# Optimization experiments

Hardware: AMD Instinct MI355X
Metric: run time of the kernel (lower is better)

## Reference

```python
import jax, jax.numpy as jnp
import numpy as np

K = 1  # number of items to sample exactly
B, N = 512, 8192


def log1mexp(x):
    # log(1 - exp(x)) for x <= 0, numerically stable (Maechler 2012)
    return jnp.where(x > -jnp.log(2.0), jnp.log(-jnp.expm1(x)), jnp.log1p(-jnp.exp(x)))


def logaddexp_c(x1, x2):
    # custom logaddexp matching the torch module (handles -inf == -inf ties)
    delta = jnp.where(x1 == x2, 0.0, x1 - x2)
    return jnp.maximum(x1, x2) + jax.nn.softplus(-jnp.abs(delta))


def dp_table(logp, logq, kk):
    # a[b, i, c] = log Pr(exactly c-1 successes among first i items); shape [B, n+1, kk+2]
    bsz = logp.shape[0]
    state0 = jnp.full((bsz, kk + 2), -jnp.inf, logp.dtype).at[:, 1].set(0.0)
    ninf_col = jnp.full((bsz, 1), -jnp.inf, logp.dtype)

    def step(state, xs):
        lp, lq = xs  # each [B]
        grown = logaddexp_c(state[:, :-1] + lp[:, None], state[:, 1:] + lq[:, None])
        new = jnp.concatenate([ninf_col, grown], axis=1)
        return new, new

    _, rows = jax.lax.scan(step, state0, (logp.T, logq.T))  # rows: [n, B, kk+2]
    return jnp.concatenate([state0[None], rows], axis=0).transpose(1, 0, 2)


def sample_scan(a, logp, noise):
    # reverse DP sampling pass; a: [B, n+1, C], logp/noise: [B, n]
    bsz, np1, C = a.shape
    n = np1 - 1
    kcol = C - 1  # == K + 1 in table-column coordinates
    ap = a[:, :-1, :][:, ::-1].transpose(1, 0, 2)  # [n, B, C], row i-1 for i=n..1
    ac = a[:, 1:, :][:, ::-1].transpose(1, 0, 2)   # [n, B, C], row i   for i=n..1
    lp_rev = logp[:, ::-1].T                        # [n, B]
    u_rev = noise[:, ::-1].T                        # [n, B]

    def step(j, xs):
        ap_r, ac_r, lp_t, u_t = xs
        p = jnp.take_along_axis(ap_r, (j - 1)[:, None], axis=1)[:, 0]
        z = jnp.take_along_axis(ac_r, j[:, None], axis=1)[:, 0]
        p = jnp.minimum(p + lp_t - z, 0.0)  # conditional log-prob, clamp fp round-off
        q = log1mexp(p)
        X = (u_t < jax.nn.sigmoid(p - q)).astype(logp.dtype)  # Bernoulli(logits=p-q)
        j = jnp.where(X > 0, j - 1, j)
        return j, X

    j0 = jnp.full((bsz,), kcol, jnp.int32)
    _, Xs = jax.lax.scan(step, j0, (ap, ac, lp_rev, u_rev))  # Xs: [n, B]
    return Xs[::-1].T  # [B, n]


def setup_inputs() -> dict:
    key = jax.random.key(0)
    k1, k2 = jax.random.split(key)
    logits = jax.random.normal(k1, (B, N), dtype=jnp.float32)
    noise = jax.random.uniform(k2, (B, N), dtype=jnp.float32)
    return {"logits": logits, "noise": noise}


def reference(logits, noise):
    logp = jnp.minimum(jax.nn.log_sigmoid(logits), -1e-7)  # clamped log_sigmoid
    logq = log1mexp(logp)
    a = dp_table(logp, logq, K)       # [B, N+1, K+2]
    return sample_scan(a, logp, noise)  # [B, N] in {0,1}
```

## Files before the change

### kernel.cpp

```cpp
#include <hip/hip_runtime.h>
#include <math.h>

#define NB 512
#define NI 8192
#define NG (NI / 4)
#define NLOG2 0.69314718055994530942f

__device__ __forceinline__ float log1mexp_f(float x) {
    return (x > -NLOG2) ? logf(-expm1f(x)) : log1pf(-expf(x));
}

__device__ int g_sel[NB];

#define TB 64
#define TK 16
__global__ __launch_bounds__(256) void prep_kernel(const float* __restrict__ logits,
                                                   float* __restrict__ Alp,
                                                   float* __restrict__ Blq) {
    __shared__ float4 lp_t[TB][TK + 1];
    __shared__ float4 lq_t[TB][TK + 1];
    int bx = blockIdx.x;
    int tb = (bx & 7) * TB;
    int tkb = (bx >> 3) * TK;
    int t = threadIdx.x;

    int kl = t & 15;
    int rl0 = t >> 4;
#pragma unroll
    for (int r = 0; r < 4; ++r) {
        int row_local = r * 16 + rl0;
        float4 x4 = *(const float4*)&logits[(size_t)(tb + row_local) * NI + (size_t)(tkb + kl) * 4];
        float4 lp4, lq4;
        const float* xs = &x4.x;
        float* lps = &lp4.x;
        float* lqs = &lq4.x;
#pragma unroll
        for (int j = 0; j < 4; ++j) {
            float x = xs[j];
            float lp = -(fmaxf(-x, 0.0f) + log1pf(expf(-fabsf(x))));
            lp = fminf(lp, -1e-7f);
            lps[j] = lp;
            lqs[j] = log1mexp_f(lp);
        }
        lp_t[row_local][kl] = lp4;
        lq_t[row_local][kl] = lq4;
    }
    __syncthreads();

    int bl = t & 63;
    int kw0 = t >> 6;
#pragma unroll
    for (int w = 0; w < 4; ++w) {
        int k_local = w * 4 + kw0;
        size_t dst = (size_t)(tkb + k_local) * NB + (size_t)(tb + bl);
        ((float4*)Alp)[dst] = lp_t[bl][k_local];
        ((float4*)Blq)[dst] = lq_t[bl][k_local];
    }
}

__device__ __forceinline__ void scan_step(float lp, float lq, float& S0, float& S1,
                                          float& x1o, float& s1o) {
    const float L2E = 1.44269504088896340736f;
    const float LN2 = 0.69314718055994530942f;
    float x1 = S0 + lp;
    float x2 = S1 + lq;
    float d  = x1 - x2;
    float m  = fmaxf(x1, x2);
    float z  = fabsf(d) * -L2E;
    float e  = __builtin_amdgcn_exp2f(z);
    float a  = 1.0f + e;
    float l  = __builtin_amdgcn_logf(a);
    S1 = fmaf(l, LN2, m);
    S0 = S0 + lq;
    x1o = x1;
    s1o = S1;
}

__device__ __forceinline__ void scan_step4(float4 lp, float4 lq, float& S0, float& S1,
                                           float4& x1v, float4& s1v) {
    scan_step(lp.x, lq.x, S0, S1, x1v.x, s1v.x);
    scan_step(lp.y, lq.y, S0, S1, x1v.y, s1v.y);
    scan_step(lp.z, lq.z, S0, S1, x1v.z, s1v.z);
    scan_step(lp.w, lq.w, S0, S1, x1v.w, s1v.w);
}

#define SD 8
__global__ __launch_bounds__(64, 1) void scan_kernel(float* __restrict__ A,
                                                     float* __restrict__ B) {
    int row = blockIdx.x * 64 + threadIdx.x;
    float4* Ap = (float4*)A;
    float4* Bp = (float4*)B;

    float S0 = 0.0f;
    float S1 = -INFINITY;

    float4 lpA[SD], lqA[SD], lpB[SD], lqB[SD];

#pragma unroll
    for (int j = 0; j < SD; ++j) {
        lpA[j] = Ap[(size_t)j * NB + row];
        lqA[j] = Bp[(size_t)j * NB + row];
    }

    const int NCHUNK = NG / SD;
    for (int c = 0; c < NCHUNK; c += 2) {
        size_t g1 = (size_t)(c + 1) * SD;
        size_t g2 = (size_t)(c + 2) * SD;

#pragma unroll
        for (int j = 0; j < SD; ++j) {
            lpB[j] = Ap[(g1 + j) * NB + row];
            lqB[j] = Bp[(g1 + j) * NB + row];
        }

#pragma unroll
        for (int j = 0; j < SD; ++j) {
            float4 x1v, s1v;
            scan_step4(lpA[j], lqA[j], S0, S1, x1v, s1v);
            size_t g = (size_t)c * SD + j;
            Ap[g * NB + row] = x1v;
            Bp[g * NB + row] = s1v;
        }

        if (c + 2 < NCHUNK) {
#pragma unroll
            for (int j = 0; j < SD; ++j) {
                lpA[j] = Ap[(g2 + j) * NB + row];
                lqA[j] = Bp[(g2 + j) * NB + row];
            }
        }

#pragma unroll
        for (int j = 0; j < SD; ++j) {
            float4 x1v, s1v;
            scan_step4(lpB[j], lqB[j], S0, S1, x1v, s1v);
            size_t g = g1 + j;
            Ap[g * NB + row] = x1v;
            Bp[g * NB + row] = s1v;
        }
    }
}

__global__ __launch_bounds__(256) void decide_kernel(const float* __restrict__ A,
                                                     const float* __restrict__ S,
                                                     const float* __restrict__ noise) {
    int row = blockIdx.x;
    const float4* x1p = (const float4*)A;
    const float4* s1p = (const float4*)S;
    const float4* ur = (const float4*)(noise + (size_t)row * NI);
    int tid = threadIdx.x;

    int best = -1;
#pragma unroll
    for (int k = 0; k < NG / 256; ++k) {
        int g = tid + k * 256;
        float4 x1 = x1p[(size_t)g * NB + row];
        float4 s1 = s1p[(size_t)g * NB + row];
        float4 u = ur[g];
#pragma unroll
        for (int j = 0; j < 4; ++j) {
            float p = fminf((&x1.x)[j] - (&s1.x)[j], 0.0f);
            float q = log1mexp_f(p);
            float z = p - q;
            float prob = 1.0f / (1.0f + expf(-z));
            if ((&u.x)[j] < prob) {
                int i = 4 * g + j;
                best = (i > best) ? i : best;
            }
        }
    }

#pragma unroll
    for (int off = 32; off > 0; off >>= 1) {
        int o = __shfl_down(best, off);
        best = (o > best) ? o : best;
    }
    __shared__ int lds[4];
    int wid = tid >> 6;
    if ((tid & 63) == 0) lds[wid] = best;
    __syncthreads();
    if (tid == 0) {
        int s01 = (lds[0] > lds[1]) ? lds[0] : lds[1];
        int s23 = (lds[2] > lds[3]) ? lds[2] : lds[3];
        g_sel[row] = (s01 > s23) ? s01 : s23;
    }
}

__global__ __launch_bounds__(256) void writeout_kernel(float* __restrict__ out) {
    int row = blockIdx.x;
    int sel = g_sel[row];
    float4* outr = (float4*)(out + (size_t)row * NI);
    int tid = threadIdx.x;
#pragma unroll
    for (int k = 0; k < NG / 256; ++k) {
        int g = tid + k * 256;
        int i0 = 4 * g;
        float4 v;
        v.x = (i0 == sel) ? 1.0f : 0.0f;
        v.y = (i0 + 1 == sel) ? 1.0f : 0.0f;
        v.z = (i0 + 2 == sel) ? 1.0f : 0.0f;
        v.w = (i0 + 3 == sel) ? 1.0f : 0.0f;
        outr[g] = v;
    }
}

extern "C" void kernel_launch(void* const* d_in, const int* in_sizes, int n_in,
                              void* d_out, int out_size, void* d_ws, size_t ws_size,
                              hipStream_t stream) {
    (void)in_sizes; (void)n_in; (void)out_size; (void)ws_size;
    const float* logits = (const float*)d_in[0];
    const float* noise = (const float*)d_in[1];
    float* out = (float*)d_out;
    float* A = (float*)d_ws;

    prep_kernel<<<8 * (NG / TK), 256, 0, stream>>>(logits, A, out);
    scan_kernel<<<8, 64, 0, stream>>>(A, out);
    decide_kernel<<<NB, 256, 0, stream>>>(A, out, noise);
    writeout_kernel<<<NB, 256, 0, stream>>>(out);
}
```

Before: 408.2 us.

## Interleave two independent row scans per thread and store only conditional log-probs

Each scan thread now handles two rows, row and row+256, and interleaves their dependent logaddexp chains so one row's latency is hidden by the other's work. The grid shrinks from 8 to 4 wavefronts. The scan also computes the clamped conditional log-prob x1 - S1 itself and writes one array instead of two, which halves scan stores and halves the decide kernel's loads. The risk is that half as many wavefronts occupy the GPU, so a latency-bound serial scan may slow down if two-way ILP does not make up for the lost parallelism.

```diff
diff --git a/kernel.cpp b/kernel.cpp
--- a/kernel.cpp
+++ b/kernel.cpp
@@ -58,8 +58,8 @@
     }
 }
 
-__device__ __forceinline__ void scan_step(float lp, float lq, float& S0, float& S1,
-                                          float& x1o, float& s1o) {
+__device__ __forceinline__ void scan_step_p(float lp, float lq, float& S0, float& S1,
+                                            float& po) {
     const float L2E = 1.44269504088896340736f;
     const float LN2 = 0.69314718055994530942f;
     float x1 = S0 + lp;
@@ -72,34 +72,29 @@
     float l  = __builtin_amdgcn_logf(a);
     S1 = fmaf(l, LN2, m);
     S0 = S0 + lq;
-    x1o = x1;
-    s1o = S1;
-}
-
-__device__ __forceinline__ void scan_step4(float4 lp, float4 lq, float& S0, float& S1,
-                                           float4& x1v, float4& s1v) {
-    scan_step(lp.x, lq.x, S0, S1, x1v.x, s1v.x);
-    scan_step(lp.y, lq.y, S0, S1, x1v.y, s1v.y);
-    scan_step(lp.z, lq.z, S0, S1, x1v.z, s1v.z);
-    scan_step(lp.w, lq.w, S0, S1, x1v.w, s1v.w);
-}
-
-#define SD 8
+    po = fminf(x1 - S1, 0.0f);
+}
+
+#define SD 4
 __global__ __launch_bounds__(64, 1) void scan_kernel(float* __restrict__ A,
                                                      float* __restrict__ B) {
     int row = blockIdx.x * 64 + threadIdx.x;
+    int row1 = row + 256;
     float4* Ap = (float4*)A;
     float4* Bp = (float4*)B;
 
-    float S0 = 0.0f;
-    float S1 = -INFINITY;
-
-    float4 lpA[SD], lqA[SD], lpB[SD], lqB[SD];
+    float S0a = 0.0f, S1a = -INFINITY;
+    float S0b = 0.0f, S1b = -INFINITY;
+
+    float4 lpA0[SD], lqA0[SD], lpA1[SD], lqA1[SD];
+    float4 lpB0[SD], lqB0[SD], lpB1[SD], lqB1[SD];
 
 #pragma unroll
     for (int j = 0; j < SD; ++j) {
-        lpA[j] = Ap[(size_t)j * NB + row];
-        lqA[j] = Bp[(size_t)j * NB + row];
+        lpA0[j] = Ap[(size_t)j * NB + row];
+        lqA0[j] = Bp[(size_t)j * NB + row];
+        lpA1[j] = Ap[(size_t)j * NB + row1];
+        lqA1[j] = Bp[(size_t)j * NB + row1];
     }
 
     const int NCHUNK = NG / SD;
@@ -109,44 +104,59 @@
 
 #pragma unroll
         for (int j = 0; j < SD; ++j) {
-            lpB[j] = Ap[(g1 + j) * NB + row];
-            lqB[j] = Bp[(g1 + j) * NB + row];
+            lpB0[j] = Ap[(g1 + j) * NB + row];
+            lqB0[j] = Bp[(g1 + j) * NB + row];
+            lpB1[j] = Ap[(g1 + j) * NB + row1];
+            lqB1[j] = Bp[(g1 + j) * NB + row1];
         }
 
 #pragma unroll
         for (int j = 0; j < SD; ++j) {
-            float4 x1v, s1v;
-            scan_step4(lpA[j], lqA[j], S0, S1, x1v, s1v);
+            float4 p0, p1;
+            scan_step_p(lpA0[j].x, lqA0[j].x, S0a, S1a, p0.x);
+            scan_step_p(lpA1[j].x, lqA1[j].x, S0b, S1b, p1.x);
+            scan_step_p(lpA0[j].y, lqA0[j].y, S0a, S1a, p0.y);
+            scan_step_p(lpA1[j].y, lqA1[j].y, S0b, S1b, p1.y);
+            scan_step_p(lpA0[j].z, lqA0[j].z, S0a, S1a, p0.z);
+            scan_step_p(lpA1[j].z, lqA1[j].z, S0b, S1b, p1.z);
+            scan_step_p(lpA0[j].w, lqA0[j].w, S0a, S1a, p0.w);
+            scan_step_p(lpA1[j].w, lqA1[j].w, S0b, S1b, p1.w);
             size_t g = (size_t)c * SD + j;
-            Ap[g * NB + row] = x1v;
-            Bp[g * NB + row] = s1v;
+            Ap[g * NB + row] = p0;
+            Ap[g * NB + row1] = p1;
         }
 
         if (c + 2 < NCHUNK) {
 #pragma unroll
             for (int j = 0; j < SD; ++j) {
-                lpA[j] = Ap[(g2 + j) * NB + row];
-                lqA[j] = Bp[(g2 + j) * NB + row];
+                lpA0[j] = Ap[(g2 + j) * NB + row];
+                lqA0[j] = Bp[(g2 + j) * NB + row];
+                lpA1[j] = Ap[(g2 + j) * NB + row1];
+                lqA1[j] = Bp[(g2 + j) * NB + row1];
             }
         }
 
 #pragma unroll
         for (int j = 0; j < SD; ++j) {
-            float4 x1v, s1v;
-            scan_step4(lpB[j], lqB[j], S0, S1, x1v, s1v);
-            size_t g = g1 + j;
-            Ap[g * NB + row] = x1v;
-            Bp[g * NB + row] = s1v;
-        }
-    }
-}
-
-__global__ __launch_bounds__(256) void decide_kernel(const float* __restrict__ A,
-                                                     const float* __restrict__ S,
+            float4 p0, p1;
+            scan_step_p(lpB0[j].x, lqB0[j].x, S0a, S1a, p0.x);
+            scan_step_p(lpB1[j].x, lqB1[j].x, S0b, S1b, p1.x);
+            scan_step_p(lpB0[j].y, lqB0[j].y, S0a, S1a, p0.y);
+            scan_step_p(lpB1[j].y, lqB1[j].y, S0b, S1b, p1.y);
+            scan_step_p(lpB0[j].z, lqB0[j].z, S0a, S1a, p0.z);
+            scan_step_p(lpB1[j].z, lqB1[j].z, S0b, S1b, p1.z);
+            scan_step_p(lpB0[j].w, lqB0[j].w, S0a, S1a, p0.w);
+            scan_step_p(lpB1[j].w, lqB1[j].w, S0b, S1b, p1.w);
+            Ap[(g1 + j) * NB + row] = p0;
+            Ap[(g1 + j) * NB + row1] = p1;
+        }
+    }
+}
+
+__global__ __launch_bounds__(256) void decide_kernel(const float* __restrict__ P,
                                                      const float* __restrict__ noise) {
     int row = blockIdx.x;
-    const float4* x1p = (const float4*)A;
-    const float4* s1p = (const float4*)S;
+    const float4* pp = (const float4*)P;
     const float4* ur = (const float4*)(noise + (size_t)row * NI);
     int tid = threadIdx.x;
 
@@ -154,12 +164,11 @@
 #pragma unroll
     for (int k = 0; k < NG / 256; ++k) {
         int g = tid + k * 256;
-        float4 x1 = x1p[(size_t)g * NB + row];
-        float4 s1 = s1p[(size_t)g * NB + row];
+        float4 p4 = pp[(size_t)g * NB + row];
         float4 u = ur[g];
 #pragma unroll
         for (int j = 0; j < 4; ++j) {
-            float p = fminf((&x1.x)[j] - (&s1.x)[j], 0.0f);
+            float p = (&p4.x)[j];
             float q = log1mexp_f(p);
             float z = p - q;
             float prob = 1.0f / (1.0f + expf(-z));
@@ -214,7 +223,7 @@
     float* A = (float*)d_ws;
 
     prep_kernel<<<8 * (NG / TK), 256, 0, stream>>>(logits, A, out);
-    scan_kernel<<<8, 64, 0, stream>>>(A, out);
-    decide_kernel<<<NB, 256, 0, stream>>>(A, out, noise);
+    scan_kernel<<<4, 64, 0, stream>>>(A, out);
+    decide_kernel<<<NB, 256, 0, stream>>>(A, noise);
     writeout_kernel<<<NB, 256, 0, stream>>>(out);
 }
```

Result: slower. 734.7 us (+80.0%).

## Emit clamped conditional log-prob from scan and fuse decide with writeout

Applied to the files above, without the earlier changes.

The scan kernel now computes the clamped conditional log-probability p = min(x1 - S1, 0) itself and writes a single float per item to a separate global buffer, instead of writing both x1 and S1 back in place. This halves the scan's store traffic and the decide kernel's loads. The writeout kernel is folded into decide, with the selected index broadcast through shared memory, which removes one launch and a global round trip. The scan also uses sched_barrier fences and wraparound prefetch indices that do redundant loads in the last iterations, and the new 16 MB device-global buffer adds memory footprint.

```diff
diff --git a/kernel.cpp b/kernel.cpp
--- a/kernel.cpp
+++ b/kernel.cpp
@@ -1,5 +1,6 @@
 #include <hip/hip_runtime.h>
 #include <math.h>
+#include <stdint.h>
 
 #define NB 512
 #define NI 8192
@@ -10,7 +11,7 @@
     return (x > -NLOG2) ? logf(-expm1f(x)) : log1pf(-expf(x));
 }
 
-__device__ int g_sel[NB];
+__device__ float g_P[(size_t)NB * NI];
 
 #define TB 64
 #define TK 16
@@ -58,8 +59,8 @@
     }
 }
 
-__device__ __forceinline__ void scan_step(float lp, float lq, float& S0, float& S1,
-                                          float& x1o, float& s1o) {
+__device__ __forceinline__ void scan_step_p(float lp, float lq, float& S0, float& S1,
+                                            float& po) {
     const float L2E = 1.44269504088896340736f;
     const float LN2 = 0.69314718055994530942f;
     float x1 = S0 + lp;
@@ -72,94 +73,93 @@
     float l  = __builtin_amdgcn_logf(a);
     S1 = fmaf(l, LN2, m);
     S0 = S0 + lq;
-    x1o = x1;
-    s1o = S1;
-}
-
-__device__ __forceinline__ void scan_step4(float4 lp, float4 lq, float& S0, float& S1,
-                                           float4& x1v, float4& s1v) {
-    scan_step(lp.x, lq.x, S0, S1, x1v.x, s1v.x);
-    scan_step(lp.y, lq.y, S0, S1, x1v.y, s1v.y);
-    scan_step(lp.z, lq.z, S0, S1, x1v.z, s1v.z);
-    scan_step(lp.w, lq.w, S0, S1, x1v.w, s1v.w);
-}
-
-#define SD 8
-__global__ __launch_bounds__(64, 1) void scan_kernel(float* __restrict__ A,
-                                                     float* __restrict__ B) {
+    po = fminf(x1 - S1, 0.0f);
+}
+
+#define CH 8
+#define SB() __builtin_amdgcn_sched_barrier(0)
+
+__global__ __launch_bounds__(64, 1) void scan_kernel(const float* __restrict__ A,
+                                                     const float* __restrict__ B) {
     int row = blockIdx.x * 64 + threadIdx.x;
-    float4* Ap = (float4*)A;
-    float4* Bp = (float4*)B;
-
-    float S0 = 0.0f;
-    float S1 = -INFINITY;
-
-    float4 lpA[SD], lqA[SD], lpB[SD], lqB[SD];
-
-#pragma unroll
-    for (int j = 0; j < SD; ++j) {
-        lpA[j] = Ap[(size_t)j * NB + row];
-        lqA[j] = Bp[(size_t)j * NB + row];
-    }
-
-    const int NCHUNK = NG / SD;
+    const float4* Ap = (const float4*)A;
+    const float4* Bp = (const float4*)B;
+    float4* Pp = (float4*)g_P;
+
+    float S0 = 0.0f, S1 = -INFINITY;
+    float4 lpE[CH], lqE[CH], lpO[CH], lqO[CH];
+
+#pragma unroll
+    for (int j = 0; j < CH; ++j) {
+        lpE[j] = Ap[(size_t)j * NB + row];
+        lqE[j] = Bp[(size_t)j * NB + row];
+    }
+#pragma unroll
+    for (int j = 0; j < CH; ++j) {
+        lpO[j] = Ap[(size_t)(CH + j) * NB + row];
+        lqO[j] = Bp[(size_t)(CH + j) * NB + row];
+    }
+
+    const int NCHUNK = NG / CH;
     for (int c = 0; c < NCHUNK; c += 2) {
-        size_t g1 = (size_t)(c + 1) * SD;
-        size_t g2 = (size_t)(c + 2) * SD;
-
-#pragma unroll
-        for (int j = 0; j < SD; ++j) {
-            lpB[j] = Ap[(g1 + j) * NB + row];
-            lqB[j] = Bp[(g1 + j) * NB + row];
-        }
-
-#pragma unroll
-        for (int j = 0; j < SD; ++j) {
-            float4 x1v, s1v;
-            scan_step4(lpA[j], lqA[j], S0, S1, x1v, s1v);
-            size_t g = (size_t)c * SD + j;
-            Ap[g * NB + row] = x1v;
-            Bp[g * NB + row] = s1v;
-        }
-
-        if (c + 2 < NCHUNK) {
-#pragma unroll
-            for (int j = 0; j < SD; ++j) {
-                lpA[j] = Ap[(g2 + j) * NB + row];
-                lqA[j] = Bp[(g2 + j) * NB + row];
+        SB();
+#pragma unroll
+        for (int j = 0; j < CH; ++j) {
+            float4 p4;
+            scan_step_p(lpE[j].x, lqE[j].x, S0, S1, p4.x);
+            scan_step_p(lpE[j].y, lqE[j].y, S0, S1, p4.y);
+            scan_step_p(lpE[j].z, lqE[j].z, S0, S1, p4.z);
+            scan_step_p(lpE[j].w, lqE[j].w, S0, S1, p4.w);
+            Pp[(size_t)(c * CH + j) * NB + row] = p4;
+        }
+        SB();
+        {
+            int g2 = ((c + 2) & (NCHUNK - 1)) * CH;
+#pragma unroll
+            for (int j = 0; j < CH; ++j) {
+                lpE[j] = Ap[(size_t)(g2 + j) * NB + row];
+                lqE[j] = Bp[(size_t)(g2 + j) * NB + row];
             }
         }
-
-#pragma unroll
-        for (int j = 0; j < SD; ++j) {
-            float4 x1v, s1v;
-            scan_step4(lpB[j], lqB[j], S0, S1, x1v, s1v);
-            size_t g = g1 + j;
-            Ap[g * NB + row] = x1v;
-            Bp[g * NB + row] = s1v;
-        }
-    }
-}
-
-__global__ __launch_bounds__(256) void decide_kernel(const float* __restrict__ A,
-                                                     const float* __restrict__ S,
-                                                     const float* __restrict__ noise) {
+        SB();
+#pragma unroll
+        for (int j = 0; j < CH; ++j) {
+            float4 p4;
+            scan_step_p(lpO[j].x, lqO[j].x, S0, S1, p4.x);
+            scan_step_p(lpO[j].y, lqO[j].y, S0, S1, p4.y);
+            scan_step_p(lpO[j].z, lqO[j].z, S0, S1, p4.z);
+            scan_step_p(lpO[j].w, lqO[j].w, S0, S1, p4.w);
+            Pp[(size_t)((c + 1) * CH + j) * NB + row] = p4;
+        }
+        SB();
+        {
+            int g3 = ((c + 3) & (NCHUNK - 1)) * CH;
+#pragma unroll
+            for (int j = 0; j < CH; ++j) {
+                lpO[j] = Ap[(size_t)(g3 + j) * NB + row];
+                lqO[j] = Bp[(size_t)(g3 + j) * NB + row];
+            }
+        }
+    }
+}
+
+__global__ __launch_bounds__(256) void decide_kernel(const float* __restrict__ noise,
+                                                     float* __restrict__ out) {
     int row = blockIdx.x;
-    const float4* x1p = (const float4*)A;
-    const float4* s1p = (const float4*)S;
+    const float4* pp = (const float4*)g_P;
     const float4* ur = (const float4*)(noise + (size_t)row * NI);
+    float4* outr = (float4*)(out + (size_t)row * NI);
     int tid = threadIdx.x;
 
     int best = -1;
 #pragma unroll
     for (int k = 0; k < NG / 256; ++k) {
         int g = tid + k * 256;
-        float4 x1 = x1p[(size_t)g * NB + row];
-        float4 s1 = s1p[(size_t)g * NB + row];
+        float4 p4 = pp[(size_t)g * NB + row];
         float4 u = ur[g];
 #pragma unroll
         for (int j = 0; j < 4; ++j) {
-            float p = fminf((&x1.x)[j] - (&s1.x)[j], 0.0f);
+            float p = (&p4.x)[j];
             float q = log1mexp_f(p);
             float z = p - q;
             float prob = 1.0f / (1.0f + expf(-z));
@@ -176,21 +176,18 @@
         best = (o > best) ? o : best;
     }
     __shared__ int lds[4];
+    __shared__ int sel_s;
     int wid = tid >> 6;
     if ((tid & 63) == 0) lds[wid] = best;
     __syncthreads();
     if (tid == 0) {
         int s01 = (lds[0] > lds[1]) ? lds[0] : lds[1];
         int s23 = (lds[2] > lds[3]) ? lds[2] : lds[3];
-        g_sel[row] = (s01 > s23) ? s01 : s23;
-    }
-}
-
-__global__ __launch_bounds__(256) void writeout_kernel(float* __restrict__ out) {
-    int row = blockIdx.x;
-    int sel = g_sel[row];
-    float4* outr = (float4*)(out + (size_t)row * NI);
-    int tid = threadIdx.x;
+        sel_s = (s01 > s23) ? s01 : s23;
+    }
+    __syncthreads();
+    int sel = sel_s;
+
 #pragma unroll
     for (int k = 0; k < NG / 256; ++k) {
         int g = tid + k * 256;
@@ -215,6 +212,5 @@
 
     prep_kernel<<<8 * (NG / TK), 256, 0, stream>>>(logits, A, out);
     scan_kernel<<<8, 64, 0, stream>>>(A, out);
-    decide_kernel<<<NB, 256, 0, stream>>>(A, out, noise);
-    writeout_kernel<<<NB, 256, 0, stream>>>(out);
-}
+    decide_kernel<<<NB, 256, 0, stream>>>(noise, out);
+}
```

After: 420.6 us. +3.0%, slower.
